# Kernel optimization log

Hardware: AMD Instinct MI355X
Metric: run time of the kernel (lower is better)

## Reference

```python
import jax, jax.numpy as jnp
import numpy as np
import itertools, math

D_K, K_BITS, L_TABLES, M_ENS = 64, 4, 8, 2
B_SZ, T_LEN, H_HEADS = 2, 512, 8


def setup_inputs() -> dict:
    key = jax.random.key(0)
    k1, k2, k3, k4 = jax.random.split(key, 4)
    shape = (M_ENS, B_SZ, T_LEN, H_HEADS, D_K)
    Khf = jax.random.normal(k1, shape, dtype=jnp.float32)
    Vhf = jax.random.normal(k2, shape, dtype=jnp.float32)
    Qhf = jax.random.normal(k3, shape, dtype=jnp.float32)
    # shared random hyperplanes: [L, K, d_k] -> [d_k, L*K]
    planes = jax.random.normal(k4, (L_TABLES, K_BITS, D_K), dtype=jnp.float32)
    planes_T = planes.reshape(L_TABLES * K_BITS, D_K).T
    # hypercube corners: [R, K] -> [K, R], R = 2**K
    corners = np.array(list(itertools.product([-1.0, 1.0], repeat=K_BITS)), dtype=np.float32)
    protos_T = jnp.asarray(corners.T)
    return {"Khf": Khf, "Vhf": Vhf, "Qhf": Qhf, "planes_T": planes_T, "protos_T": protos_T}


def reference(Khf, Vhf, Qhf, planes_T, protos_T):
    M, B, T, H, dk = Khf.shape
    K = protos_T.shape[0]
    L = planes_T.shape[1] // K
    scale = math.sqrt(dk)
    N = M * B * H

    # [M,B,T,H,dk] -> [N,T,dk] with N = M*B*H (heads folded next to batch)
    def fold(x):
        return jnp.transpose(x, (0, 1, 3, 2, 4)).reshape(N, T, dk)

    Kh2, Qh2, V2 = fold(Khf), fold(Qhf), fold(Vhf)

    # random-hyperplane projections -> per-table softmax over 2**K corners
    def probs(x):
        proj = (x @ planes_T).reshape(N, T, L, K)          # [N,T,L,K]
        logits = jnp.einsum('ntlk,kr->ntlr', jnp.tanh(proj) / scale, protos_T)
        return jax.nn.softmax(logits, axis=-1)             # [N,T,L,R]

    probsK = probs(Kh2)
    probsQ = probs(Qh2)

    # causal prefix sums (linear-attention style state)
    A_pref = jnp.cumsum(probsK, axis=1)                    # [N,T,L,R]
    B_pref = jnp.cumsum(probsK[..., None] * V2[:, :, None, None, :], axis=1)  # [N,T,L,R,dk]
    E_pref = B_pref / (A_pref[..., None] + 1e-6)

    out2 = jnp.einsum('ntlr,ntlrd->ntd', probsQ, E_pref)   # [N,T,dk]
    out = out2.reshape(M, B, H, T, dk).transpose(0, 1, 3, 2, 4)
    return out
```

## Files before the change

kernel.cpp:

```cpp
#include <hip/hip_runtime.h>
#include <hip/hip_bf16.h>
#include <math.h>

#define T_LEN 512
#define H_HEADS 8
#define DK 64
#define LR 128
#define NTOT 32

typedef __attribute__((ext_vector_type(8))) short bf16x8;
typedef __attribute__((ext_vector_type(4))) float f32x4;

__device__ __forceinline__ float fast_tanh(float x) {
    float e = __expf(2.0f * x);
    return 1.0f - 2.0f / (1.0f + e);
}

__device__ __forceinline__ unsigned f2bf(float x) {
    union { float f; unsigned u; } v; v.f = x;
    unsigned r = v.u + 0x7FFF + ((v.u >> 16) & 1);
    return r >> 16;
}

__device__ __forceinline__ float bflo(unsigned u) {
    union { unsigned u; float f; } v; v.u = u << 16; return v.f;
}
__device__ __forceinline__ float bfhi(unsigned u) {
    union { unsigned u; float f; } v; v.u = u & 0xFFFF0000u; return v.f;
}

__global__ __launch_bounds__(256) void k_probs(
    const float* __restrict__ Khf, const float* __restrict__ Qhf,
    const float* __restrict__ Vhf,
    const float* __restrict__ planesT, const float* __restrict__ protosT,
    unsigned short* __restrict__ pKB, unsigned short* __restrict__ pKt,
    unsigned short* __restrict__ pQB, unsigned short* __restrict__ VBT,
    float* __restrict__ Spart)
{
    __shared__ __align__(16) unsigned char smraw[39040];
    short* Psh    = (short*)smraw;
    float* protos = (float*)(smraw + 4608);
    short* Xsh    = (short*)(smraw + 4864);
    float* xt     = (float*)(smraw + 9472);
    float* pbuf   = (float*)(smraw + 13696);
    float* vb     = (float*)(smraw + 30592);

    const int bx = blockIdx.x;
    const int n  = bx & 31;
    const int u  = bx >> 5;
    const int tile = u >> 1;
    const int side = u & 1;
    const int t0 = tile * 32;
    const int g  = n >> 3, h = n & 7;
    const int tid = threadIdx.x;
    const int wv = tid >> 6, lane = tid & 63, m16 = lane & 15, q = lane >> 4;

    {
        int d = tid >> 2, jb = (tid & 3) * 8;
        float4 a = *(const float4*)(planesT + d * 32 + jb);
        float4 b = *(const float4*)(planesT + d * 32 + jb + 4);
        float pv[8] = {a.x, a.y, a.z, a.w, b.x, b.y, b.z, b.w};
#pragma unroll
        for (int i = 0; i < 8; ++i)
            Psh[(jb + i) * 72 + d] = (short)f2bf(pv[i]);
    }
    if (tid < 64) protos[tid] = protosT[tid];
    {
        int row = tid >> 3, seg = tid & 7;
        const float* src = (side ? Qhf : Khf) +
            ((long)(g * T_LEN + t0 + row) * H_HEADS + h) * DK + seg * 8;
        float4 a = *(const float4*)src;
        float4 b = *(const float4*)(src + 4);
        uint4 uu;
        uu.x = f2bf(a.x) | (f2bf(a.y) << 16);
        uu.y = f2bf(a.z) | (f2bf(a.w) << 16);
        uu.z = f2bf(b.x) | (f2bf(b.y) << 16);
        uu.w = f2bf(b.z) | (f2bf(b.w) << 16);
        *(uint4*)(Xsh + row * 72 + seg * 8) = uu;
    }
    __syncthreads();

    {
        const int mb = wv & 1, nb = wv >> 1;
        f32x4 s = (f32x4){0.f, 0.f, 0.f, 0.f};
#pragma unroll
        for (int ks = 0; ks < 2; ++ks) {
            bf16x8 af = *(const bf16x8*)(Xsh + (mb * 16 + m16) * 72 + ks * 32 + q * 8);
            bf16x8 bf = *(const bf16x8*)(Psh + (nb * 16 + m16) * 72 + ks * 32 + q * 8);
            s = __builtin_amdgcn_mfma_f32_16x16x32_bf16(af, bf, s, 0, 0, 0);
        }
#pragma unroll
        for (int p = 0; p < 4; ++p)
            xt[(mb * 16 + q * 4 + p) * 33 + nb * 16 + m16] =
                fast_tanh(s[p]) * 0.125f;
    }
    __syncthreads();

    const int r = tid & 15, l = (tid >> 4) & 7, thi = tid >> 7;
    {
        float p0 = protos[r], p1 = protos[16 + r], p2 = protos[32 + r], p3 = protos[48 + r];
#pragma unroll 4
        for (int w = 0; w < 16; ++w) {
            int tl = w * 2 + thi;
            const float* x = xt + tl * 33 + l * 4;
            float logit = x[0] * p0 + x[1] * p1 + x[2] * p2 + x[3] * p3;
            float e = __expf(logit);
            float s = e;
            s += __shfl_xor(s, 1, 16);
            s += __shfl_xor(s, 2, 16);
            s += __shfl_xor(s, 4, 16);
            s += __shfl_xor(s, 8, 16);
            pbuf[(l * 16 + r) * 33 + tl] = e / s;
        }
    }
    if (side) {
#pragma unroll
        for (int it = 0; it < 2; ++it) {
            int fid = it * 256 + tid;
            int t = fid >> 4, c4 = fid & 15;
            float4 v = *(const float4*)(Vhf + ((size_t)(g * T_LEN + t0 + t) * H_HEADS + h) * DK + c4 * 4);
            vb[(c4 * 4 + 0) * 33 + t] = v.x;
            vb[(c4 * 4 + 1) * 33 + t] = v.y;
            vb[(c4 * 4 + 2) * 33 + t] = v.z;
            vb[(c4 * 4 + 3) * 33 + t] = v.w;
        }
    }
    __syncthreads();

    if (side == 0) {
        unsigned* dst = (unsigned*)pKB;
#pragma unroll
        for (int it = 0; it < 8; ++it) {
            int fid = it * 256 + tid;
            int lr = fid >> 4, tp2 = fid & 15;
            unsigned u0 = f2bf(pbuf[lr * 33 + tp2 * 2]);
            unsigned u1 = f2bf(pbuf[lr * 33 + tp2 * 2 + 1]);
            dst[(size_t)(n * LR + lr) * 256 + tile * 16 + tp2] = u0 | (u1 << 16);
        }
        unsigned* dt = (unsigned*)pKt + (size_t)n * 32768 + t0 * 64;
#pragma unroll
        for (int it = 0; it < 8; ++it) {
            int fid = it * 256 + tid;
            int t = fid >> 6, lrp = fid & 63;
            unsigned u0 = f2bf(pbuf[(2 * lrp) * 33 + t]);
            unsigned u1 = f2bf(pbuf[(2 * lrp + 1) * 33 + t]);
            dt[t * 64 + lrp] = u0 | (u1 << 16);
        }
        {
            int lr = tid >> 1, hf = tid & 1;
            float s = 0.f;
            const float* row = pbuf + lr * 33 + hf * 16;
#pragma unroll
            for (int t = 0; t < 16; ++t) s += row[t];
            s += __shfl_xor(s, 1, 2);
            if (!hf) Spart[((size_t)n * 16 + tile) * 128 + lr] = s;
        }
    } else {
        unsigned* dst = (unsigned*)pQB;
#pragma unroll
        for (int it = 0; it < 8; ++it) {
            int fid = it * 256 + tid;
            int lr = fid >> 4, tp2 = fid & 15;
            unsigned u0 = f2bf(pbuf[lr * 33 + tp2 * 2]);
            unsigned u1 = f2bf(pbuf[lr * 33 + tp2 * 2 + 1]);
            dst[(size_t)(n * LR + lr) * 256 + tile * 16 + tp2] = u0 | (u1 << 16);
        }
        unsigned* dstv = (unsigned*)VBT + (size_t)n * 16384;
#pragma unroll
        for (int it = 0; it < 4; ++it) {
            int fid = it * 256 + tid;
            int d = fid >> 4, tp2 = fid & 15;
            unsigned u0 = f2bf(vb[d * 33 + tp2 * 2]);
            unsigned u1 = f2bf(vb[d * 33 + tp2 * 2 + 1]);
            dstv[d * 256 + tile * 16 + tp2] = u0 | (u1 << 16);
        }
    }
}

__global__ __launch_bounds__(1024) void k_attn(
    const unsigned short* __restrict__ pKB, const unsigned short* __restrict__ pKt,
    const unsigned short* __restrict__ pQB, const unsigned short* __restrict__ VBT,
    const float* __restrict__ Spart, float* __restrict__ out)
{
    __shared__ __align__(16) short sm[71680];
    const int n = blockIdx.x & 31, rt = blockIdx.x >> 5;
    const int g = n >> 3, h = n & 7;
    const int tid = threadIdx.x;
    const int wave = tid >> 6, wg = wave >> 2, w = wave & 3;
    const int lane = tid & 63, m16 = lane & 15, q = lane >> 4;
    const int gtid = tid & 255;

    short* Ksh = sm + wg * 8704;
    short* Vsh = sm + 34816 + wg * 4608;
    short* Ssh = sm + 53248 + wg * 4608;
    short* Qsh = sm;

    {
        const int s8 = lane & 7;
        const int lr = wave * 8 + (lane >> 3);
        float bsum = 0.f;
        for (int j = 0; j < 2 * rt; ++j)
            bsum += Spart[((size_t)n * 16 + j) * 128 + lr];
        uint4 ku = *(const uint4*)(pKB + ((size_t)n * LR + lr) * 512 + rt * 64 + s8 * 8);
        unsigned kuu[4] = {ku.x, ku.y, ku.z, ku.w};
        float s[8];
        s[0] = bflo(kuu[0]);        s[1] = s[0] + bfhi(kuu[0]);
        s[2] = s[1] + bflo(kuu[1]); s[3] = s[2] + bfhi(kuu[1]);
        s[4] = s[3] + bflo(kuu[2]); s[5] = s[4] + bfhi(kuu[2]);
        s[6] = s[5] + bflo(kuu[3]); s[7] = s[6] + bfhi(kuu[3]);
        float tot = s[7];
#pragma unroll
        for (int off = 1; off < 8; off <<= 1) {
            float v = __shfl_up(tot, off, 8);
            if (s8 >= off) tot += v;
        }
        float base = bsum + tot - s[7];
        uint4 qu = *(const uint4*)(pQB + ((size_t)n * LR + lr) * 512 + rt * 64 + s8 * 8);
        unsigned quu[4] = {qu.x, qu.y, qu.z, qu.w};
        float qf[8] = {bflo(quu[0]), bfhi(quu[0]), bflo(quu[1]), bfhi(quu[1]),
                       bflo(quu[2]), bfhi(quu[2]), bflo(quu[3]), bfhi(quu[3])};
        const int qbase = ((wave ^ s8) << 3) + (lr & 7);
#pragma unroll
        for (int i = 0; i < 8; ++i)
            Qsh[(s8 * 8 + i) * 136 + qbase] = (short)f2bf(qf[i] / (base + s[i] + 1e-6f));
    }
    __syncthreads();

    bf16x8 qa[4];
    {
        const int row = w * 16 + m16, rk = row >> 3;
#pragma unroll
        for (int st = 0; st < 4; ++st)
            qa[st] = *(const bf16x8*)(Qsh + row * 136 + (((st * 4 + q) ^ rk) << 3));
    }

    const unsigned short* kt = pKt + (size_t)n * 65536;
    const unsigned short* kv = VBT + (size_t)n * 32768;
    uint4 pk[4], pv[2];
    auto pref = [&](int c) {
#pragma unroll
        for (int it = 0; it < 4; ++it) {
            int fid = it * 256 + gtid;
            pk[it] = *(const uint4*)(kt + (size_t)(c * 64 + (fid >> 4)) * 128 + (fid & 15) * 8);
        }
#pragma unroll
        for (int it = 0; it < 2; ++it) {
            int fid = it * 256 + gtid;
            pv[it] = *(const uint4*)(kv + (size_t)(fid >> 3) * 512 + c * 64 + (fid & 7) * 8);
        }
    };

    f32x4 o[4];
    o[0] = o[1] = o[2] = o[3] = (f32x4){0.f, 0.f, 0.f, 0.f};

    if (wg <= rt) pref(wg);
    const int rounds = (rt >> 2) + 1;
    for (int r0 = 0; r0 < rounds; ++r0) {
        const int c = r0 * 4 + wg;
        const bool act = (c <= rt);
        __syncthreads();
        if (act) {
#pragma unroll
            for (int it = 0; it < 4; ++it) {
                int fid = it * 256 + gtid;
                *(uint4*)(Ksh + (fid >> 4) * 136 + (fid & 15) * 8) = pk[it];
            }
            *(uint4*)(Vsh + (gtid >> 3) * 72 + (gtid & 7) * 8) = pv[0];
            *(uint4*)(Vsh + ((gtid + 256) >> 3) * 72 + (gtid & 7) * 8) = pv[1];
        }
        __syncthreads();
        if (c + 4 <= rt) pref(c + 4);
        if (act) {
            f32x4 s[4];
            s[0] = s[1] = s[2] = s[3] = (f32x4){0.f, 0.f, 0.f, 0.f};
#pragma unroll
            for (int st = 0; st < 4; ++st)
#pragma unroll
                for (int nb = 0; nb < 4; ++nb) {
                    bf16x8 b = *(const bf16x8*)(Ksh + (nb * 16 + m16) * 136 + st * 32 + q * 8);
                    s[nb] = __builtin_amdgcn_mfma_f32_16x16x32_bf16(qa[st], b, s[nb], 0, 0, 0);
                }
            if (c == rt) {
#pragma unroll
                for (int nb = 0; nb < 4; ++nb)
#pragma unroll
                    for (int p = 0; p < 4; ++p)
                        if (nb * 16 + m16 > w * 16 + q * 4 + p) s[nb][p] = 0.f;
            }
#pragma unroll
            for (int nb = 0; nb < 4; ++nb)
#pragma unroll
                for (int p = 0; p < 4; ++p) {
                    union { float f; unsigned u; } cv; cv.f = s[nb][p];
                    Ssh[(w * 16 + q * 4 + p) * 72 + nb * 16 + m16] =
                        (short)((cv.u + 0x8000u) >> 16);
                }
#pragma unroll
            for (int st = 0; st < 2; ++st) {
                bf16x8 a = *(const bf16x8*)(Ssh + (w * 16 + m16) * 72 + st * 32 + q * 8);
#pragma unroll
                for (int nb = 0; nb < 4; ++nb) {
                    bf16x8 b = *(const bf16x8*)(Vsh + (nb * 16 + m16) * 72 + st * 32 + q * 8);
                    o[nb] = __builtin_amdgcn_mfma_f32_16x16x32_bf16(a, b, o[nb], 0, 0, 0);
                }
            }
        }
    }

    __syncthreads();
    float* Obuf = (float*)sm;
    if (wg) {
        float* ob = Obuf + (wg - 1) * 4352;
#pragma unroll
        for (int nb = 0; nb < 4; ++nb)
#pragma unroll
            for (int p = 0; p < 4; ++p)
                ob[(w * 16 + q * 4 + p) * 68 + nb * 16 + m16] = o[nb][p];
    }
    __syncthreads();
    if (wg == 0) {
        float* dst = out + ((size_t)(g * T_LEN + rt * 64 + w * 16 + q * 4) * H_HEADS + h) * DK;
#pragma unroll
        for (int p = 0; p < 4; ++p)
#pragma unroll
            for (int nb = 0; nb < 4; ++nb) {
                int idx = (w * 16 + q * 4 + p) * 68 + nb * 16 + m16;
                dst[p * (H_HEADS * DK) + nb * 16 + m16] =
                    o[nb][p] + Obuf[idx] + Obuf[4352 + idx] + Obuf[8704 + idx];
            }
    }
}

extern "C" void kernel_launch(void* const* d_in, const int* in_sizes, int n_in,
                              void* d_out, int out_size, void* d_ws, size_t ws_size,
                              hipStream_t stream) {
    const float* Khf     = (const float*)d_in[0];
    const float* Vhf     = (const float*)d_in[1];
    const float* Qhf     = (const float*)d_in[2];
    const float* planesT = (const float*)d_in[3];
    const float* protosT = (const float*)d_in[4];
    float* outp = (float*)d_out;

    const size_t NE = (size_t)NTOT * LR * T_LEN;
    unsigned short* pKB = (unsigned short*)d_ws;
    unsigned short* pKt = pKB + NE;
    unsigned short* pQB = pKt + NE;
    unsigned short* VBT = pQB + NE;
    float* Spart = (float*)(VBT + (size_t)NTOT * DK * T_LEN);

    k_probs<<<dim3(1024), dim3(256), 0, stream>>>(
        Khf, Qhf, Vhf, planesT, protosT, pKB, pKt, pQB, VBT, Spart);
    k_attn<<<dim3(256), dim3(1024), 0, stream>>>(pKB, pKt, pQB, VBT, Spart, outp);
}
```

Measured before the change: 102.9 us.

## Factorize hypercube-corner softmax into per-bit sigmoids and write transposed probs from registers

Replaces the 16-way softmax over hypercube-corner logits with a product of four per-bit sigmoids. This holds because the logit is a sum of independent ±x_k terms. It cuts the exps, shuffle reductions and divides per table to four exps and a few multiplies. It also drops the protos input and its shared-memory staging. The transposed K-probability buffer is now packed to bf16 and stored straight from registers as 16-byte writes, removing a separate shared-memory re-read pass. The risk is that the code now assumes the corner matrix uses itertools.product ordering rather than reading it from input.

```diff
diff --git a/kernel.cpp b/kernel.cpp
--- a/kernel.cpp
+++ b/kernel.cpp
@@ -31,15 +31,13 @@
 
 __global__ __launch_bounds__(256) void k_probs(
     const float* __restrict__ Khf, const float* __restrict__ Qhf,
-    const float* __restrict__ Vhf,
-    const float* __restrict__ planesT, const float* __restrict__ protosT,
+    const float* __restrict__ Vhf, const float* __restrict__ planesT,
     unsigned short* __restrict__ pKB, unsigned short* __restrict__ pKt,
     unsigned short* __restrict__ pQB, unsigned short* __restrict__ VBT,
     float* __restrict__ Spart)
 {
     __shared__ __align__(16) unsigned char smraw[39040];
     short* Psh    = (short*)smraw;
-    float* protos = (float*)(smraw + 4608);
     short* Xsh    = (short*)(smraw + 4864);
     float* xt     = (float*)(smraw + 9472);
     float* pbuf   = (float*)(smraw + 13696);
@@ -64,7 +62,6 @@
         for (int i = 0; i < 8; ++i)
             Psh[(jb + i) * 72 + d] = (short)f2bf(pv[i]);
     }
-    if (tid < 64) protos[tid] = protosT[tid];
     {
         int row = tid >> 3, seg = tid & 7;
         const float* src = (side ? Qhf : Khf) +
@@ -96,21 +93,40 @@
     }
     __syncthreads();
 
-    const int r = tid & 15, l = (tid >> 4) & 7, thi = tid >> 7;
-    {
-        float p0 = protos[r], p1 = protos[16 + r], p2 = protos[32 + r], p3 = protos[48 + r];
-#pragma unroll 4
-        for (int w = 0; w < 16; ++w) {
-            int tl = w * 2 + thi;
-            const float* x = xt + tl * 33 + l * 4;
-            float logit = x[0] * p0 + x[1] * p1 + x[2] * p2 + x[3] * p3;
-            float e = __expf(logit);
-            float s = e;
-            s += __shfl_xor(s, 1, 16);
-            s += __shfl_xor(s, 2, 16);
-            s += __shfl_xor(s, 4, 16);
-            s += __shfl_xor(s, 8, 16);
-            pbuf[(l * 16 + r) * 33 + tl] = e / s;
+    {
+        const int tl = tid & 31, l = tid >> 5;
+        const float* x = xt + tl * 33 + l * 4;
+        float P[4], M[4];
+#pragma unroll
+        for (int k = 0; k < 4; ++k) {
+            float e = __expf(-2.0f * x[k]);
+            float inv = 1.0f / (1.0f + e);
+            P[k] = inv; M[k] = e * inv;
+        }
+        float ab[4] = {M[0]*M[1], M[0]*P[1], P[0]*M[1], P[0]*P[1]};
+        float cd[4] = {M[2]*M[3], M[2]*P[3], P[2]*M[3], P[2]*P[3]};
+        float* pb = pbuf + (l * 16) * 33 + tl;
+        unsigned w0x, w0y, w0z, w0w, w1x, w1y, w1z, w1w;
+        float pr[16];
+#pragma unroll
+        for (int r = 0; r < 16; ++r) {
+            pr[r] = ab[r >> 2] * cd[r & 3];
+            pb[r * 33] = pr[r];
+        }
+        if (side == 0) {
+            w0x = f2bf(pr[0])  | (f2bf(pr[1])  << 16);
+            w0y = f2bf(pr[2])  | (f2bf(pr[3])  << 16);
+            w0z = f2bf(pr[4])  | (f2bf(pr[5])  << 16);
+            w0w = f2bf(pr[6])  | (f2bf(pr[7])  << 16);
+            w1x = f2bf(pr[8])  | (f2bf(pr[9])  << 16);
+            w1y = f2bf(pr[10]) | (f2bf(pr[11]) << 16);
+            w1z = f2bf(pr[12]) | (f2bf(pr[13]) << 16);
+            w1w = f2bf(pr[14]) | (f2bf(pr[15]) << 16);
+            unsigned short* dt = pKt + (size_t)n * 65536 + (size_t)(t0 + tl) * 128 + l * 16;
+            uint4 a; a.x = w0x; a.y = w0y; a.z = w0z; a.w = w0w;
+            uint4 b; b.x = w1x; b.y = w1y; b.z = w1z; b.w = w1w;
+            *(uint4*)dt       = a;
+            *(uint4*)(dt + 8) = b;
         }
     }
     if (side) {
@@ -136,15 +152,6 @@
             unsigned u0 = f2bf(pbuf[lr * 33 + tp2 * 2]);
             unsigned u1 = f2bf(pbuf[lr * 33 + tp2 * 2 + 1]);
             dst[(size_t)(n * LR + lr) * 256 + tile * 16 + tp2] = u0 | (u1 << 16);
-        }
-        unsigned* dt = (unsigned*)pKt + (size_t)n * 32768 + t0 * 64;
-#pragma unroll
-        for (int it = 0; it < 8; ++it) {
-            int fid = it * 256 + tid;
-            int t = fid >> 6, lrp = fid & 63;
-            unsigned u0 = f2bf(pbuf[(2 * lrp) * 33 + t]);
-            unsigned u1 = f2bf(pbuf[(2 * lrp + 1) * 33 + t]);
-            dt[t * 64 + lrp] = u0 | (u1 << 16);
         }
         {
             int lr = tid >> 1, hf = tid & 1;
@@ -338,7 +345,6 @@
     const float* Vhf     = (const float*)d_in[1];
     const float* Qhf     = (const float*)d_in[2];
     const float* planesT = (const float*)d_in[3];
-    const float* protosT = (const float*)d_in[4];
     float* outp = (float*)d_out;
 
     const size_t NE = (size_t)NTOT * LR * T_LEN;
@@ -349,6 +355,6 @@
     float* Spart = (float*)(VBT + (size_t)NTOT * DK * T_LEN);
 
     k_probs<<<dim3(1024), dim3(256), 0, stream>>>(
-        Khf, Qhf, Vhf, planesT, protosT, pKB, pKt, pQB, VBT, Spart);
+        Khf, Qhf, Vhf, planesT, pKB, pKt, pQB, VBT, Spart);
     k_attn<<<dim3(256), dim3(1024), 0, stream>>>(pKB, pKt, pQB, VBT, Spart, outp);
 }
```

New measurement: 96.49 us. 1.07x faster.
